# Performance work log

Hardware: AMD Instinct MI355X
Metric: run time of the kernel (lower is better)

Reference implementation:

```python
import jax, jax.numpy as jnp
import numpy as np

BLOCKSIZE = 4096  # bnb quantize_blockwise default; chunk_size asserted % 4096 == 0


def dequantize_blockwise(quant_weight, absmax, code):
    """Dequantize int8 codes: w = code[q] * absmax[block], blocks of 4096 over flat tensor."""
    V, D = quant_weight.shape
    vals = code[quant_weight.reshape(-1)]                 # [V*D] fp32 codebook lookup
    vals = vals.reshape(-1, BLOCKSIZE) * absmax[:, None]  # per-block absmax scale
    return vals.reshape(V, D)


def setup_inputs() -> dict:
    key = jax.random.key(0)
    k1, k2, k3, k4 = jax.random.split(key, 4)
    V, D = 50304, 1024
    n_blocks = (V * D) // BLOCKSIZE  # 12576
    x = jax.random.randint(k1, (8, 2048), 0, V, dtype=jnp.int64)
    quant_weight = jax.random.randint(k2, (V, D), 0, 256, dtype=jnp.int32)
    absmax = jax.random.uniform(k3, (n_blocks,), dtype=jnp.float32)
    code = jax.random.normal(k4, (256,), dtype=jnp.float32)
    return {"x": x, "quant_weight": quant_weight, "absmax": absmax, "code": code}


def reference(x, quant_weight, absmax, code):
    table = dequantize_blockwise(quant_weight, absmax, code)  # [V, D] fp32
    return table[x]                                           # [B, S, D] embedding gather
```

## Files before the change

### kernel.cpp

```cpp
#include <hip/hip_runtime.h>
#include <hip/hip_bf16.h>


__global__ __launch_bounds__(256) void qembed_kernel(
    const int* __restrict__ x,
    const int* __restrict__ qw,
    const float* __restrict__ absmax,
    const float* __restrict__ code,
    float* __restrict__ out,
    int D)
{
    __shared__ float lcode[256];
    lcode[threadIdx.x] = code[threadIdx.x];
    __syncthreads();

    const int row = blockIdx.x;
    const int v = x[row];
    const long long base = (long long)v * (long long)D;
    const long long obase = (long long)row * (long long)D;

    for (int d = threadIdx.x * 4; d < D; d += 256 * 4) {
        const float am = absmax[(base + d) >> 12];

        const int4 q = *reinterpret_cast<const int4*>(qw + base + d);

        float4 o;
        o.x = lcode[q.x & 0xFF] * am;
        o.y = lcode[q.y & 0xFF] * am;
        o.z = lcode[q.z & 0xFF] * am;
        o.w = lcode[q.w & 0xFF] * am;

        *reinterpret_cast<float4*>(out + obase + d) = o;
    }
}

extern "C" void kernel_launch(void* const* d_in, const int* in_sizes, int n_in,
                              void* d_out, int out_size, void* d_ws, size_t ws_size,
                              hipStream_t stream) {
    const int*   x      = (const int*)d_in[0];
    const int*   qw     = (const int*)d_in[1];
    const float* absmax = (const float*)d_in[2];
    const float* code   = (const float*)d_in[3];
    float*       out    = (float*)d_out;

    const int n_rows = in_sizes[0];
    const int D = out_size / n_rows;

    qembed_kernel<<<n_rows, 256, 0, stream>>>(x, qw, absmax, code, out, D);
}
```

Before: 273.9 us.

## Process eight rows per block with batched loads and nontemporal stores

Each block now handles eight embedding rows, issuing all eight quantized-row loads and absmax loads before any compute so more memory requests are in flight per thread. Output writes use nontemporal stores to avoid polluting the cache with write-only data. The grid shrinks eightfold, which cuts block launch and codebook-staging overhead but lowers the number of blocks and raises register use per thread. The inner loop assumes D is a multiple of 1024.

New measurement: 276.3 us. Within noise of the previous version (+0.9%).

```diff
diff --git a/kernel.cpp b/kernel.cpp
--- a/kernel.cpp
+++ b/kernel.cpp
@@ -1,6 +1,10 @@
 #include <hip/hip_runtime.h>
 #include <hip/hip_bf16.h>
 
+
+typedef float v4f __attribute__((ext_vector_type(4)));
+
+#define ROWS_PER_BLOCK 8
 
 __global__ __launch_bounds__(256) void qembed_kernel(
     const int* __restrict__ x,
@@ -8,29 +12,46 @@
     const float* __restrict__ absmax,
     const float* __restrict__ code,
     float* __restrict__ out,
-    int D)
+    int n_rows, int D)
 {
     __shared__ float lcode[256];
+    __shared__ int lidx[ROWS_PER_BLOCK];
+
     lcode[threadIdx.x] = code[threadIdx.x];
+
+    const int row0 = blockIdx.x * ROWS_PER_BLOCK;
+    if (threadIdx.x < ROWS_PER_BLOCK) {
+        int r = row0 + threadIdx.x;
+        lidx[threadIdx.x] = (r < n_rows) ? x[r] : 0;
+    }
     __syncthreads();
 
-    const int row = blockIdx.x;
-    const int v = x[row];
-    const long long base = (long long)v * (long long)D;
-    const long long obase = (long long)row * (long long)D;
+    const int tid = threadIdx.x;
 
-    for (int d = threadIdx.x * 4; d < D; d += 256 * 4) {
-        const float am = absmax[(base + d) >> 12];
+    for (int dbase = 0; dbase < D; dbase += 1024) {
+        int4  q[ROWS_PER_BLOCK];
+        float am[ROWS_PER_BLOCK];
 
-        const int4 q = *reinterpret_cast<const int4*>(qw + base + d);
+#pragma unroll
+        for (int i = 0; i < ROWS_PER_BLOCK; ++i) {
+            const int v = __builtin_amdgcn_readfirstlane(lidx[i]);
+            const long long base = (long long)v * (long long)D + dbase;
+            am[i] = absmax[base >> 12];
+            q[i]  = *reinterpret_cast<const int4*>(qw + base + tid * 4);
+        }
 
-        float4 o;
-        o.x = lcode[q.x & 0xFF] * am;
-        o.y = lcode[q.y & 0xFF] * am;
-        o.z = lcode[q.z & 0xFF] * am;
-        o.w = lcode[q.w & 0xFF] * am;
-
-        *reinterpret_cast<float4*>(out + obase + d) = o;
+#pragma unroll
+        for (int i = 0; i < ROWS_PER_BLOCK; ++i) {
+            const int r = row0 + i;
+            if (r >= n_rows) break;
+            v4f o;
+            o.x = lcode[q[i].x & 0xFF] * am[i];
+            o.y = lcode[q[i].y & 0xFF] * am[i];
+            o.z = lcode[q[i].z & 0xFF] * am[i];
+            o.w = lcode[q[i].w & 0xFF] * am[i];
+            v4f* dst = reinterpret_cast<v4f*>(out + (long long)r * D + dbase + tid * 4);
+            __builtin_nontemporal_store(o, dst);
+        }
     }
 }
 
@@ -46,5 +67,6 @@
     const int n_rows = in_sizes[0];
     const int D = out_size / n_rows;
 
-    qembed_kernel<<<n_rows, 256, 0, stream>>>(x, qw, absmax, code, out, D);
+    const int grid = (n_rows + ROWS_PER_BLOCK - 1) / ROWS_PER_BLOCK;
+    qembed_kernel<<<grid, 256, 0, stream>>>(x, qw, absmax, code, out, n_rows, D);
 }
```
